# Kernel tuning notes

Measured on AMD Instinct MI355X. Metric: run time of the kernel, lower is better.

The kernel has to match this reference:

```python
import jax, jax.numpy as jnp
import numpy as np

NUM_HEADS = 12
DIM = 768
HEAD_DIM = DIM // NUM_HEADS
NUM_BUCKETS = 32
MAX_DISTANCE = 128
ELEV_SCALE = 1000.0


def _bucket_positions(relative_position):
    # Faithful port of RelativePositionBias2D._bucket_positions (torch .long() truncates;
    # values passed through the large branch are non-negative so astype(int32) matches).
    nb = NUM_BUCKETS // 2  # 16
    n = -relative_position
    ret = (n < 0).astype(jnp.int32) * nb
    n = jnp.abs(n)
    max_exact = nb // 2  # 8
    is_small = n < max_exact
    n_safe = jnp.maximum(n, 1).astype(jnp.float32)  # avoid log(0); masked by is_small
    val_if_large = max_exact + (
        jnp.log(n_safe / max_exact) / np.float32(np.log(MAX_DISTANCE / max_exact)) * (nb - max_exact)
    ).astype(jnp.int32)
    val_if_large = jnp.minimum(val_if_large, nb - 1)
    return ret + jnp.where(is_small, n, val_if_large)


def _bucket_idx(coords_2d):
    # coords_2d: [B, N, 2] in [0,1] -> integer grid coords
    coords_int = (coords_2d * MAX_DISTANCE).astype(jnp.int32)
    rel_x = coords_int[:, :, None, 0] - coords_int[:, None, :, 0]  # [B,N,N]
    rel_y = coords_int[:, :, None, 1] - coords_int[:, None, :, 1]
    bx = _bucket_positions(rel_x)
    by = _bucket_positions(rel_y)
    return bx * NUM_BUCKETS + by  # [B,N,N] int32 in [0, 1024)


def setup_inputs() -> dict:
    key = jax.random.key(0)
    ks = jax.random.split(key, 8)
    B, N, D = 4, 1024, DIM
    x = jax.random.normal(ks[0], (B, N, D), dtype=jnp.float32)
    coords_2d = jax.random.uniform(ks[1], (B, N, 2), dtype=jnp.float32)
    elevation_patches = jax.random.normal(ks[2], (B, N), dtype=jnp.float32) * 2000.0  # meters
    qkv_w = jax.random.normal(ks[3], (3 * D, D), dtype=jnp.float32) * 0.02
    qkv_b = jnp.zeros((3 * D,), dtype=jnp.float32)
    proj_w = jax.random.normal(ks[4], (D, D), dtype=jnp.float32) * 0.02
    proj_b = jnp.zeros((D,), dtype=jnp.float32)
    bias_table = jax.random.normal(ks[5], (NUM_BUCKETS * NUM_BUCKETS, NUM_HEADS), dtype=jnp.float32) * 0.02
    alpha = jnp.full((1,), 2.0, dtype=jnp.float32)
    return {"x": x, "coords_2d": coords_2d, "elevation_patches": elevation_patches,
            "qkv_w": qkv_w, "qkv_b": qkv_b, "proj_w": proj_w, "proj_b": proj_b,
            "bias_table": bias_table, "alpha": alpha}


def reference(x, coords_2d, elevation_patches, qkv_w, qkv_b, proj_w, proj_b, bias_table, alpha):
    B, N, D = x.shape
    H, hd = NUM_HEADS, HEAD_DIM
    scale = hd ** -0.5

    qkv = x @ qkv_w.T + qkv_b  # [B,N,3D]
    qkv = qkv.reshape(B, N, 3, H, hd)
    q = qkv[:, :, 0].transpose(0, 2, 1, 3)  # [B,H,N,hd]
    k = qkv[:, :, 1].transpose(0, 2, 1, 3)
    v = qkv[:, :, 2].transpose(0, 2, 1, 3)

    attn = jnp.einsum('bhnd,bhmd->bhnm', q * scale, k)  # [B,H,N,N]

    # relative position bias: gather from table, [B,N,N,H] -> [B,H,N,N]
    idx = _bucket_idx(coords_2d)
    rel_bias = bias_table[idx].transpose(0, 3, 1, 2)
    attn = attn + rel_bias

    # elevation bias: [B,N,N], broadcast over heads
    elev_diff = (elevation_patches[:, None, :] - elevation_patches[:, :, None]) / ELEV_SCALE
    elev_bias = jnp.clip(-alpha[0] * jax.nn.relu(elev_diff), -10.0, 0.0)
    attn = attn + elev_bias[:, None, :, :]

    attn = jax.nn.softmax(attn.astype(jnp.float32), axis=-1).astype(q.dtype)

    out = jnp.einsum('bhnm,bhmd->bhnd', attn, v)  # [B,H,N,hd]
    out = out.transpose(0, 2, 1, 3).reshape(B, N, D)
    return out @ proj_w.T + proj_b
```

## Files before the change

kernel.cpp:

```cpp
#include <hip/hip_runtime.h>
#include <hip/hip_bf16.h>
#include <math.h>

#define NH 12
#define HD 64
#define NSEQ 1024
#define DMODEL 768
#define LOG2E 1.44269504f

#if defined(__has_builtin)
#if __has_builtin(__builtin_amdgcn_permlane32_swap) && __has_builtin(__builtin_amdgcn_permlane16_swap)
#define USE_PLSWAP 1
#endif
#endif

typedef unsigned short ushort_t;
typedef float f32x4 __attribute__((ext_vector_type(4)));
typedef short bf16x8 __attribute__((ext_vector_type(8)));

__device__ __forceinline__ ushort_t f2bf(float f) {
    unsigned int u = __float_as_uint(f);
    u += 0x7FFFu + ((u >> 16) & 1u);
    return (ushort_t)(u >> 16);
}

__device__ __forceinline__ unsigned pk2(float x, float y) {
    __hip_bfloat162 t = __float22bfloat162_rn(make_float2(x, y));
    union { __hip_bfloat162 b; unsigned u; } c; c.b = t;
    return c.u;
}

__device__ __forceinline__ void gl_lds16(const ushort_t* g, ushort_t* l) {
    __builtin_amdgcn_global_load_lds(
        (const __attribute__((address_space(1))) unsigned int*)g,
        (__attribute__((address_space(3))) unsigned int*)l, 16, 0, 0);
}

#define XB_N   3145728u
#define WQB_N  1769472u
#define PWB_N  589824u
#define CVT_BLOCKS 2688

__device__ __forceinline__ int bucketf(int rel) {
    const int n = -rel;
    const int u = (n < 0) ? 16 : 0;
    const int a = n < 0 ? -n : n;
    if (a < 8) return u + a;
    int v = 8 + (int)(log2f((float)a * 0.125f) * 2.0f + 1e-4f);
    if (v > 15) v = 15;
    return u + v;
}

__global__ __launch_bounds__(256) void prep_kernel(
    const float* __restrict__ x, const float* __restrict__ w1,
    const float* __restrict__ w2, ushort_t* __restrict__ dst,
    const float* __restrict__ coords, const float* __restrict__ elev,
    const float* __restrict__ alpha_p, unsigned* __restrict__ pack)
{
    const int t = threadIdx.x;
    if (blockIdx.x < CVT_BLOCKS) {
        const unsigned i = blockIdx.x * 256 + t;
        const unsigned n0 = XB_N / 8, n1 = n0 + WQB_N / 8, n2 = n1 + PWB_N / 8;
        if (i >= n2) return;
        const float* src; unsigned off;
        if (i < n0)      { src = x;  off = i; }
        else if (i < n1) { src = w1; off = i - n0; }
        else             { src = w2; off = i - n1; }
        const float4 a = ((const float4*)src)[off * 2];
        const float4 b = ((const float4*)src)[off * 2 + 1];
        uint4 pk;
        pk.x = pk2(a.x, a.y); pk.y = pk2(a.z, a.w);
        pk.z = pk2(b.x, b.y); pk.w = pk2(b.z, b.w);
        ((uint4*)dst)[i] = pk;
    } else {
        const int blk = blockIdx.x - CVT_BLOCKS;
        const int b = blk >> 10, i = blk & 1023;
        const float alpha = alpha_p[0];
        const float2 ci = *(const float2*)&coords[(size_t)(b * NSEQ + i) * 2];
        const int cxi = (int)(ci.x * 128.0f), cyi = (int)(ci.y * 128.0f);
        const float ei = elev[b * NSEQ + i];
        const int j0 = t * 4;
        const float4 c01 = *(const float4*)&coords[(size_t)(b * NSEQ + j0) * 2];
        const float4 c23 = *(const float4*)&coords[(size_t)(b * NSEQ + j0 + 2) * 2];
        const float4 ej4 = *(const float4*)&elev[b * NSEQ + j0];
        const float cjx[4] = {c01.x, c01.z, c23.x, c23.z};
        const float cjy[4] = {c01.y, c01.w, c23.y, c23.w};
        const float ejv[4] = {ej4.x, ej4.y, ej4.z, ej4.w};
        unsigned r[4];
        #pragma unroll
        for (int k = 0; k < 4; ++k) {
            const int bx = bucketf(cxi - (int)(cjx[k] * 128.0f));
            const int by = bucketf(cyi - (int)(cjy[k] * 128.0f));
            const int idx = (bx << 5) + by;
            const float ed = (ejv[k] - ei) * 1e-3f;
            const float eb = fmaxf(-alpha * fmaxf(ed, 0.0f), -10.0f) * LOG2E;
            r[k] = ((unsigned)f2bf(eb) << 16) | (unsigned)idx;
        }
        uint4 o; o.x = r[0]; o.y = r[1]; o.z = r[2]; o.w = r[3];
        *(uint4*)&pack[((size_t)b << 20) + (size_t)i * NSEQ + j0] = o;
    }
}

__global__ __launch_bounds__(256) void qkv_gemm(
    const ushort_t* __restrict__ A, const ushort_t* __restrict__ B,
    const float* __restrict__ bias,
    ushort_t* __restrict__ Qb, ushort_t* __restrict__ Kb, ushort_t* __restrict__ Vtb)
{
    __shared__ __align__(16) ushort_t SM[6144];
    ushort_t* Asb = SM;
    ushort_t* Bsb = SM + 4096;
    const int t = threadIdx.x;
    const int lane = t & 63, w = t >> 6;
    const int wr = w >> 1, wc = w & 1;
    const int col = lane & 15, quad = lane >> 4;
    const int m0 = blockIdx.y * 128, c0 = blockIdx.x * 64;

    const f32x4 zero = {0.f, 0.f, 0.f, 0.f};
    f32x4 acc[4][2];
    #pragma unroll
    for (int i = 0; i < 4; ++i)
        #pragma unroll
        for (int j = 0; j < 2; ++j) acc[i][j] = zero;

    const int arow = w * 32 + (lane >> 2);
    const int brow = w * 16 + (lane >> 2);
    const int scol = (lane & 3) * 8;
    const ushort_t* Ag = A + (size_t)(m0 + arow) * DMODEL + scol;
    const ushort_t* Bg = B + (size_t)(c0 + brow) * DMODEL + scol;
    ushort_t* Asw = Asb + w * 32 * 32;
    ushort_t* Bsw = Bsb + w * 16 * 32;

    for (int k0 = 0; k0 < DMODEL; k0 += 32) {
        __syncthreads();
        gl_lds16(Ag + k0, Asw);
        gl_lds16(Ag + (size_t)16 * DMODEL + k0, Asw + 16 * 32);
        gl_lds16(Bg + k0, Bsw);
        __syncthreads();
        bf16x8 af[4], bf[2];
        #pragma unroll
        for (int im = 0; im < 4; ++im)
            af[im] = *(const bf16x8*)&Asb[(wr * 64 + im * 16 + col) * 32 + quad * 8];
        #pragma unroll
        for (int jn = 0; jn < 2; ++jn)
            bf[jn] = *(const bf16x8*)&Bsb[(wc * 32 + jn * 16 + col) * 32 + quad * 8];
        #pragma unroll
        for (int im = 0; im < 4; ++im)
            #pragma unroll
            for (int jn = 0; jn < 2; ++jn)
                acc[im][jn] = __builtin_amdgcn_mfma_f32_16x16x32_bf16(af[im], bf[jn], acc[im][jn], 0, 0, 0);
    }

    const int s = c0 / DMODEL;
    const int h = (c0 % DMODEL) >> 6;
    const int b = m0 >> 10;
    const int bh = b * NH + h;
    const int n0 = (m0 & (NSEQ - 1)) + wr * 64;
    const int d0 = (c0 & 63);
    const int cb = c0 + wc * 32;

    __syncthreads();

    if (s < 2) {
        ushort_t* lt = SM + w * 1280;
        ushort_t* dst = (s == 0) ? Qb : Kb;
        const float sc = (s == 0) ? 0.125f * LOG2E : 1.0f;
        float bv[2];
        #pragma unroll
        for (int jn = 0; jn < 2; ++jn) bv[jn] = bias[cb + jn * 16 + col];
        const int row16 = lane >> 2, seg = lane & 3;
        #pragma unroll
        for (int im = 0; im < 4; ++im) {
            #pragma unroll
            for (int jn = 0; jn < 2; ++jn) {
                const f32x4 a = acc[im][jn];
                #pragma unroll
                for (int r = 0; r < 4; ++r)
                    lt[(quad * 4 + r) * 40 + jn * 16 + col] = f2bf((a[r] + bv[jn]) * sc);
            }
            const uint4 u0 = *(const uint4*)&lt[row16 * 40 + seg * 8];
            const size_t gb = ((size_t)bh * NSEQ + n0 + im * 16 + row16) * HD
                            + wc * 32 + seg * 8;
            *(uint4*)&dst[gb] = u0;
        }
    } else {
        #pragma unroll
        for (int im = 0; im < 4; ++im) {
            #pragma unroll
            for (int jn = 0; jn < 2; ++jn) {
                const int d = wc * 32 + jn * 16 + col;
                const float bvv = bias[cb + jn * 16 + col];
                const f32x4 a = acc[im][jn];
                uint2 p;
                p.x = pk2(a[0] + bvv, a[1] + bvv);
                p.y = pk2(a[2] + bvv, a[3] + bvv);
                *(uint2*)&Vtb[((size_t)bh * HD + d) * NSEQ + n0 + im * 16 + quad * 4] = p;
            }
        }
    }
    (void)d0;
}

__global__ __launch_bounds__(256) void attn_mfma(
    const ushort_t* __restrict__ Qb, const ushort_t* __restrict__ Kb,
    const ushort_t* __restrict__ Vtb,
    const unsigned* __restrict__ pack,
    const float* __restrict__ table,
    ushort_t* __restrict__ Ob)
{
    __shared__ __align__(16) ushort_t Ks[2][64 * 72];
    __shared__ __align__(16) ushort_t Vt[2][64 * 72];
#if !USE_PLSWAP
    __shared__ __align__(16) ushort_t Ps[64 * 72];
#endif
    __shared__ ushort_t tabu[1024];

    const int t = threadIdx.x;
    const int lane = t & 63, w = t >> 6;
    const int col = lane & 15, quad = lane >> 4;
    const int bid = blockIdx.x;
    const int it = bid & 15, bh = bid >> 4;
    const int h = bh % NH, b = bh / NH;
    const int i0 = it * 64;

    for (int i = t; i < 1024; i += 256)
        tabu[i] = f2bf(table[i * NH + h] * LOG2E);

    const ushort_t* Qg = Qb + ((size_t)bh * NSEQ + i0 + w * 16 + col) * HD;
    const bf16x8 aq0 = *(const bf16x8*)(Qg + quad * 8);
    const bf16x8 aq1 = *(const bf16x8*)(Qg + 32 + quad * 8);

    const size_t kvbase = (size_t)bh * NSEQ * HD;
    const unsigned* prow = pack + ((size_t)b << 20)
                         + (size_t)(i0 + w * 16 + col) * NSEQ + quad * 4;

    const int srow = t >> 3, sc8 = (t & 7) * 8;
    const int so0 = srow * 72 + sc8;
    const int so1 = (srow + 32) * 72 + sc8;

    uint4 k0 = *(const uint4*)&Kb[kvbase + (size_t)srow * HD + sc8];
    uint4 k1 = *(const uint4*)&Kb[kvbase + (size_t)(srow + 32) * HD + sc8];
    uint4 v0 = *(const uint4*)&Vtb[kvbase + (size_t)srow * NSEQ + sc8];
    uint4 v1 = *(const uint4*)&Vtb[kvbase + (size_t)(srow + 32) * NSEQ + sc8];
    *(uint4*)&Ks[0][so0] = k0;
    *(uint4*)&Ks[0][so1] = k1;
    *(uint4*)&Vt[0][so0] = v0;
    *(uint4*)&Vt[0][so1] = v1;
    k0 = *(const uint4*)&Kb[kvbase + (size_t)(64 + srow) * HD + sc8];
    k1 = *(const uint4*)&Kb[kvbase + (size_t)(64 + srow + 32) * HD + sc8];
    v0 = *(const uint4*)&Vtb[kvbase + (size_t)srow * NSEQ + 64 + sc8];
    v1 = *(const uint4*)&Vtb[kvbase + (size_t)(srow + 32) * NSEQ + 64 + sc8];

    const f32x4 zero = {0.f, 0.f, 0.f, 0.f};
    f32x4 o_acc[4];
    #pragma unroll
    for (int i = 0; i < 4; ++i) o_acc[i] = zero;
    float l_l = 0.f;

    #pragma unroll 2
    for (int jt = 0; jt < 16; ++jt) {
        __syncthreads();
        const int cur = jt & 1;
        const int j0 = jt * 64;

        if (jt < 15) {
            *(uint4*)&Ks[cur ^ 1][so0] = k0;
            *(uint4*)&Ks[cur ^ 1][so1] = k1;
            *(uint4*)&Vt[cur ^ 1][so0] = v0;
            *(uint4*)&Vt[cur ^ 1][so1] = v1;
        }
        if (jt < 14) {
            const int j2 = (jt + 2) * 64;
            k0 = *(const uint4*)&Kb[kvbase + (size_t)(j2 + srow) * HD + sc8];
            k1 = *(const uint4*)&Kb[kvbase + (size_t)(j2 + srow + 32) * HD + sc8];
            v0 = *(const uint4*)&Vtb[kvbase + (size_t)srow * NSEQ + j2 + sc8];
            v1 = *(const uint4*)&Vtb[kvbase + (size_t)(srow + 32) * NSEQ + j2 + sc8];
        }
        uint4 pk4[4];
        #pragma unroll
        for (int jb = 0; jb < 4; ++jb)
            pk4[jb] = *(const uint4*)(prow + j0 + jb * 16);

        f32x4 sacc[4];
        #pragma unroll
        for (int jb = 0; jb < 4; ++jb) {
            sacc[jb] = zero;
            const bf16x8 kb0 = *(const bf16x8*)&Ks[cur][(jb * 16 + col) * 72 + quad * 8];
            const bf16x8 kb1 = *(const bf16x8*)&Ks[cur][(jb * 16 + col) * 72 + 32 + quad * 8];
            sacc[jb] = __builtin_amdgcn_mfma_f32_16x16x32_bf16(kb0, aq0, sacc[jb], 0, 0, 0);
            sacc[jb] = __builtin_amdgcn_mfma_f32_16x16x32_bf16(kb1, aq1, sacc[jb], 0, 0, 0);
        }

        float rbeb[4][4];
        #pragma unroll
        for (int jb = 0; jb < 4; ++jb) {
            const uint4 pkv = pk4[jb];
            rbeb[jb][0] = __uint_as_float((unsigned)tabu[pkv.x & 1023u] << 16) + __uint_as_float(pkv.x & 0xFFFF0000u);
            rbeb[jb][1] = __uint_as_float((unsigned)tabu[pkv.y & 1023u] << 16) + __uint_as_float(pkv.y & 0xFFFF0000u);
            rbeb[jb][2] = __uint_as_float((unsigned)tabu[pkv.z & 1023u] << 16) + __uint_as_float(pkv.z & 0xFFFF0000u);
            rbeb[jb][3] = __uint_as_float((unsigned)tabu[pkv.w & 1023u] << 16) + __uint_as_float(pkv.w & 0xFFFF0000u);
        }

        float psum = 0.f;
        unsigned Wd[4][2];
        #pragma unroll
        for (int jb = 0; jb < 4; ++jb) {
            const float p0 = exp2f(sacc[jb][0] + rbeb[jb][0]);
            const float p1 = exp2f(sacc[jb][1] + rbeb[jb][1]);
            const float p2 = exp2f(sacc[jb][2] + rbeb[jb][2]);
            const float p3 = exp2f(sacc[jb][3] + rbeb[jb][3]);
            psum += (p0 + p1) + (p2 + p3);
            Wd[jb][0] = pk2(p0, p1);
            Wd[jb][1] = pk2(p2, p3);
        }
        l_l += psum;

        bf16x8 ap0, ap1;
#if USE_PLSWAP
        {
            union { unsigned u[4]; bf16x8 b; } A0, A1;
            #pragma unroll
            for (int j1 = 0; j1 < 2; ++j1) {
                #pragma unroll
                for (int v = 0; v < 2; ++v) {
                    auto h1 = __builtin_amdgcn_permlane32_swap(
                        Wd[2 * j1][v], Wd[2 * j1 + 1][v], false, false);
                    auto h2 = __builtin_amdgcn_permlane16_swap(
                        h1[0], h1[1], false, false);
                    if (j1 == 0) { A0.u[0 + v] = h2[0]; A0.u[2 + v] = h2[1]; }
                    else         { A1.u[0 + v] = h2[0]; A1.u[2 + v] = h2[1]; }
                }
            }
            ap0 = A0.b;
            ap1 = A1.b;
        }
#else
        #pragma unroll
        for (int jb = 0; jb < 4; ++jb) {
            uint2 st;
            st.x = Wd[jb][0];
            st.y = Wd[jb][1];
            *(uint2*)&Ps[(w * 16 + col) * 72 + jb * 16 + quad * 4] = st;
        }
        ap0 = *(const bf16x8*)&Ps[(w * 16 + col) * 72 + quad * 8];
        ap1 = *(const bf16x8*)&Ps[(w * 16 + col) * 72 + 32 + quad * 8];
#endif

        #pragma unroll
        for (int db = 0; db < 4; ++db) {
            const bf16x8 vv0 = *(const bf16x8*)&Vt[cur][(db * 16 + col) * 72 + quad * 8];
            const bf16x8 vv1 = *(const bf16x8*)&Vt[cur][(db * 16 + col) * 72 + 32 + quad * 8];
            o_acc[db] = __builtin_amdgcn_mfma_f32_16x16x32_bf16(ap0, vv0, o_acc[db], 0, 0, 0);
            o_acc[db] = __builtin_amdgcn_mfma_f32_16x16x32_bf16(ap1, vv1, o_acc[db], 0, 0, 0);
        }
    }

    float l = l_l;
    l += __shfl_xor(l, 16);
    l += __shfl_xor(l, 32);
    #pragma unroll
    for (int r = 0; r < 4; ++r) {
        const float lr = __shfl(l, w * 16 + quad * 4 + r);
        const float inv = 1.f / lr;
        const int ri = w * 16 + quad * 4 + r;
        const size_t base = ((size_t)(b * NSEQ) + i0 + ri) * DMODEL + h * HD;
        #pragma unroll
        for (int db = 0; db < 4; ++db)
            Ob[base + db * 16 + col] = f2bf(o_acc[db][r] * inv);
    }
}

__global__ __launch_bounds__(256) void proj_gemm(
    const ushort_t* __restrict__ A, const ushort_t* __restrict__ B,
    const float* __restrict__ bias, float* __restrict__ out)
{
    __shared__ __align__(16) ushort_t As[64 * 32];
    __shared__ __align__(16) ushort_t Bs[64 * 32];
    const int t = threadIdx.x;
    const int lane = t & 63, w = t >> 6;
    const int wr = w >> 1, wc = w & 1;
    const int col = lane & 15, quad = lane >> 4;
    const int m0 = blockIdx.y * 64, c0 = blockIdx.x * 64;

    const f32x4 zero = {0.f, 0.f, 0.f, 0.f};
    f32x4 acc[2][2];
    #pragma unroll
    for (int i = 0; i < 2; ++i)
        #pragma unroll
        for (int j = 0; j < 2; ++j) acc[i][j] = zero;

    const int srow = w * 16 + (lane >> 2);
    const int scol = (lane & 3) * 8;
    const ushort_t* Ag = A + (size_t)(m0 + srow) * DMODEL + scol;
    const ushort_t* Bg = B + (size_t)(c0 + srow) * DMODEL + scol;
    ushort_t* Asw = &As[w * 16 * 32];
    ushort_t* Bsw = &Bs[w * 16 * 32];

    for (int k0 = 0; k0 < DMODEL; k0 += 32) {
        __syncthreads();
        gl_lds16(Ag + k0, Asw);
        gl_lds16(Bg + k0, Bsw);
        __syncthreads();
        bf16x8 af[2], bf[2];
        #pragma unroll
        for (int im = 0; im < 2; ++im)
            af[im] = *(const bf16x8*)&As[(wr * 32 + im * 16 + col) * 32 + quad * 8];
        #pragma unroll
        for (int jn = 0; jn < 2; ++jn)
            bf[jn] = *(const bf16x8*)&Bs[(wc * 32 + jn * 16 + col) * 32 + quad * 8];
        #pragma unroll
        for (int im = 0; im < 2; ++im)
            #pragma unroll
            for (int jn = 0; jn < 2; ++jn)
                acc[im][jn] = __builtin_amdgcn_mfma_f32_16x16x32_bf16(af[im], bf[jn], acc[im][jn], 0, 0, 0);
    }

    #pragma unroll
    for (int im = 0; im < 2; ++im) {
        #pragma unroll
        for (int jn = 0; jn < 2; ++jn) {
            const int c = c0 + wc * 32 + jn * 16 + col;
            const float bv = bias[c];
            #pragma unroll
            for (int r = 0; r < 4; ++r) {
                const int m = m0 + wr * 32 + im * 16 + quad * 4 + r;
                out[(size_t)m * DMODEL + c] = acc[im][jn][r] + bv;
            }
        }
    }
}

extern "C" void kernel_launch(void* const* d_in, const int* in_sizes, int n_in,
                              void* d_out, int out_size, void* d_ws, size_t ws_size,
                              hipStream_t stream) {
    const float* x       = (const float*)d_in[0];
    const float* coords  = (const float*)d_in[1];
    const float* elev    = (const float*)d_in[2];
    const float* qkv_w   = (const float*)d_in[3];
    const float* qkv_b   = (const float*)d_in[4];
    const float* proj_w  = (const float*)d_in[5];
    const float* proj_b  = (const float*)d_in[6];
    const float* btable  = (const float*)d_in[7];
    const float* alpha   = (const float*)d_in[8];
    float* out = (float*)d_out;

    ushort_t* wsu = (ushort_t*)d_ws;
    ushort_t* xb  = wsu;
    ushort_t* wqb = wsu + 3145728;
    ushort_t* pwb = wsu + 4915200;
    ushort_t* Qb  = wsu + 5505024;
    ushort_t* Kb  = wsu + 8650752;
    ushort_t* Vtb = wsu + 11796480;
    ushort_t* Ob  = wsu + 14942208;
    unsigned* pck = (unsigned*)(wsu + 18087936);

    prep_kernel<<<CVT_BLOCKS + 4096, 256, 0, stream>>>(
        x, qkv_w, proj_w, wsu, coords, elev, alpha, pck);
    qkv_gemm<<<dim3(36, 32), 256, 0, stream>>>(xb, wqb, qkv_b, Qb, Kb, Vtb);
    attn_mfma<<<768, 256, 0, stream>>>(Qb, Kb, Vtb, pck, btable, Ob);
    proj_gemm<<<dim3(12, 64), 256, 0, stream>>>(Ob, pwb, proj_b, out);
}
```

Before: 191.8 us.

## Split attention key range across two wave groups per block with LDS reduction

The attention kernel now launches 512 threads per block. Two groups of four waves each process half of the key/value sequence for the same 64 query rows, using their own double-buffered LDS tiles. At the end, the partial outputs and row sums are combined through LDS before normalisation. The goal is more waves in flight and a shorter serial loop per wave, in exchange for more LDS, an extra reduction step and dropping the non-permlane fallback path.

```diff
diff --git a/kernel.cpp b/kernel.cpp
--- a/kernel.cpp
+++ b/kernel.cpp
@@ -7,12 +7,6 @@
 #define NSEQ 1024
 #define DMODEL 768
 #define LOG2E 1.44269504f
-
-#if defined(__has_builtin)
-#if __has_builtin(__builtin_amdgcn_permlane32_swap) && __has_builtin(__builtin_amdgcn_permlane16_swap)
-#define USE_PLSWAP 1
-#endif
-#endif
 
 typedef unsigned short ushort_t;
 typedef float f32x4 __attribute__((ext_vector_type(4)));
@@ -200,55 +194,55 @@
     (void)d0;
 }
 
-__global__ __launch_bounds__(256) void attn_mfma(
+__global__ __launch_bounds__(512) void attn_mfma(
     const ushort_t* __restrict__ Qb, const ushort_t* __restrict__ Kb,
     const ushort_t* __restrict__ Vtb,
     const unsigned* __restrict__ pack,
     const float* __restrict__ table,
     ushort_t* __restrict__ Ob)
 {
-    __shared__ __align__(16) ushort_t Ks[2][64 * 72];
-    __shared__ __align__(16) ushort_t Vt[2][64 * 72];
-#if !USE_PLSWAP
-    __shared__ __align__(16) ushort_t Ps[64 * 72];
-#endif
+    __shared__ __align__(16) ushort_t Ks[2][2][64 * 72];
+    __shared__ __align__(16) ushort_t Vt[2][2][64 * 72];
     __shared__ ushort_t tabu[1024];
 
     const int t = threadIdx.x;
     const int lane = t & 63, w = t >> 6;
+    const int g = w >> 2, wg = w & 3;
     const int col = lane & 15, quad = lane >> 4;
     const int bid = blockIdx.x;
     const int it = bid & 15, bh = bid >> 4;
     const int h = bh % NH, b = bh / NH;
     const int i0 = it * 64;
 
-    for (int i = t; i < 1024; i += 256)
+    for (int i = t; i < 1024; i += 512)
         tabu[i] = f2bf(table[i * NH + h] * LOG2E);
 
-    const ushort_t* Qg = Qb + ((size_t)bh * NSEQ + i0 + w * 16 + col) * HD;
+    const ushort_t* Qg = Qb + ((size_t)bh * NSEQ + i0 + wg * 16 + col) * HD;
     const bf16x8 aq0 = *(const bf16x8*)(Qg + quad * 8);
     const bf16x8 aq1 = *(const bf16x8*)(Qg + 32 + quad * 8);
 
     const size_t kvbase = (size_t)bh * NSEQ * HD;
     const unsigned* prow = pack + ((size_t)b << 20)
-                         + (size_t)(i0 + w * 16 + col) * NSEQ + quad * 4;
-
-    const int srow = t >> 3, sc8 = (t & 7) * 8;
+                         + (size_t)(i0 + wg * 16 + col) * NSEQ + quad * 4;
+
+    const int tg = t & 255;
+    const int srow = tg >> 3, sc8 = (tg & 7) * 8;
     const int so0 = srow * 72 + sc8;
     const int so1 = (srow + 32) * 72 + sc8;
-
-    uint4 k0 = *(const uint4*)&Kb[kvbase + (size_t)srow * HD + sc8];
-    uint4 k1 = *(const uint4*)&Kb[kvbase + (size_t)(srow + 32) * HD + sc8];
-    uint4 v0 = *(const uint4*)&Vtb[kvbase + (size_t)srow * NSEQ + sc8];
-    uint4 v1 = *(const uint4*)&Vtb[kvbase + (size_t)(srow + 32) * NSEQ + sc8];
-    *(uint4*)&Ks[0][so0] = k0;
-    *(uint4*)&Ks[0][so1] = k1;
-    *(uint4*)&Vt[0][so0] = v0;
-    *(uint4*)&Vt[0][so1] = v1;
-    k0 = *(const uint4*)&Kb[kvbase + (size_t)(64 + srow) * HD + sc8];
-    k1 = *(const uint4*)&Kb[kvbase + (size_t)(64 + srow + 32) * HD + sc8];
-    v0 = *(const uint4*)&Vtb[kvbase + (size_t)srow * NSEQ + 64 + sc8];
-    v1 = *(const uint4*)&Vtb[kvbase + (size_t)(srow + 32) * NSEQ + 64 + sc8];
+    const int r0 = g * 512;
+
+    uint4 k0 = *(const uint4*)&Kb[kvbase + (size_t)(r0 + srow) * HD + sc8];
+    uint4 k1 = *(const uint4*)&Kb[kvbase + (size_t)(r0 + srow + 32) * HD + sc8];
+    uint4 v0 = *(const uint4*)&Vtb[kvbase + (size_t)srow * NSEQ + r0 + sc8];
+    uint4 v1 = *(const uint4*)&Vtb[kvbase + (size_t)(srow + 32) * NSEQ + r0 + sc8];
+    *(uint4*)&Ks[g][0][so0] = k0;
+    *(uint4*)&Ks[g][0][so1] = k1;
+    *(uint4*)&Vt[g][0][so0] = v0;
+    *(uint4*)&Vt[g][0][so1] = v1;
+    k0 = *(const uint4*)&Kb[kvbase + (size_t)(r0 + 64 + srow) * HD + sc8];
+    k1 = *(const uint4*)&Kb[kvbase + (size_t)(r0 + 64 + srow + 32) * HD + sc8];
+    v0 = *(const uint4*)&Vtb[kvbase + (size_t)srow * NSEQ + r0 + 64 + sc8];
+    v1 = *(const uint4*)&Vtb[kvbase + (size_t)(srow + 32) * NSEQ + r0 + 64 + sc8];
 
     const f32x4 zero = {0.f, 0.f, 0.f, 0.f};
     f32x4 o_acc[4];
@@ -257,19 +251,19 @@
     float l_l = 0.f;
 
     #pragma unroll 2
-    for (int jt = 0; jt < 16; ++jt) {
+    for (int s = 0; s < 8; ++s) {
         __syncthreads();
-        const int cur = jt & 1;
-        const int j0 = jt * 64;
-
-        if (jt < 15) {
-            *(uint4*)&Ks[cur ^ 1][so0] = k0;
-            *(uint4*)&Ks[cur ^ 1][so1] = k1;
-            *(uint4*)&Vt[cur ^ 1][so0] = v0;
-            *(uint4*)&Vt[cur ^ 1][so1] = v1;
-        }
-        if (jt < 14) {
-            const int j2 = (jt + 2) * 64;
+        const int cur = s & 1;
+        const int j0 = r0 + s * 64;
+
+        if (s < 7) {
+            *(uint4*)&Ks[g][cur ^ 1][so0] = k0;
+            *(uint4*)&Ks[g][cur ^ 1][so1] = k1;
+            *(uint4*)&Vt[g][cur ^ 1][so0] = v0;
+            *(uint4*)&Vt[g][cur ^ 1][so1] = v1;
+        }
+        if (s < 6) {
+            const int j2 = r0 + (s + 2) * 64;
             k0 = *(const uint4*)&Kb[kvbase + (size_t)(j2 + srow) * HD + sc8];
             k1 = *(const uint4*)&Kb[kvbase + (size_t)(j2 + srow + 32) * HD + sc8];
             v0 = *(const uint4*)&Vtb[kvbase + (size_t)srow * NSEQ + j2 + sc8];
@@ -284,8 +278,8 @@
         #pragma unroll
         for (int jb = 0; jb < 4; ++jb) {
             sacc[jb] = zero;
-            const bf16x8 kb0 = *(const bf16x8*)&Ks[cur][(jb * 16 + col) * 72 + quad * 8];
-            const bf16x8 kb1 = *(const bf16x8*)&Ks[cur][(jb * 16 + col) * 72 + 32 + quad * 8];
+            const bf16x8 kb0 = *(const bf16x8*)&Ks[g][cur][(jb * 16 + col) * 72 + quad * 8];
+            const bf16x8 kb1 = *(const bf16x8*)&Ks[g][cur][(jb * 16 + col) * 72 + 32 + quad * 8];
             sacc[jb] = __builtin_amdgcn_mfma_f32_16x16x32_bf16(kb0, aq0, sacc[jb], 0, 0, 0);
             sacc[jb] = __builtin_amdgcn_mfma_f32_16x16x32_bf16(kb1, aq1, sacc[jb], 0, 0, 0);
         }
@@ -315,7 +309,6 @@
         l_l += psum;
 
         bf16x8 ap0, ap1;
-#if USE_PLSWAP
         {
             union { unsigned u[4]; bf16x8 b; } A0, A1;
             #pragma unroll
@@ -333,22 +326,11 @@
             ap0 = A0.b;
             ap1 = A1.b;
         }
-#else
-        #pragma unroll
-        for (int jb = 0; jb < 4; ++jb) {
-            uint2 st;
-            st.x = Wd[jb][0];
-            st.y = Wd[jb][1];
-            *(uint2*)&Ps[(w * 16 + col) * 72 + jb * 16 + quad * 4] = st;
-        }
-        ap0 = *(const bf16x8*)&Ps[(w * 16 + col) * 72 + quad * 8];
-        ap1 = *(const bf16x8*)&Ps[(w * 16 + col) * 72 + 32 + quad * 8];
-#endif
 
         #pragma unroll
         for (int db = 0; db < 4; ++db) {
-            const bf16x8 vv0 = *(const bf16x8*)&Vt[cur][(db * 16 + col) * 72 + quad * 8];
-            const bf16x8 vv1 = *(const bf16x8*)&Vt[cur][(db * 16 + col) * 72 + 32 + quad * 8];
+            const bf16x8 vv0 = *(const bf16x8*)&Vt[g][cur][(db * 16 + col) * 72 + quad * 8];
+            const bf16x8 vv1 = *(const bf16x8*)&Vt[g][cur][(db * 16 + col) * 72 + 32 + quad * 8];
             o_acc[db] = __builtin_amdgcn_mfma_f32_16x16x32_bf16(ap0, vv0, o_acc[db], 0, 0, 0);
             o_acc[db] = __builtin_amdgcn_mfma_f32_16x16x32_bf16(ap1, vv1, o_acc[db], 0, 0, 0);
         }
@@ -357,15 +339,32 @@
     float l = l_l;
     l += __shfl_xor(l, 16);
     l += __shfl_xor(l, 32);
-    #pragma unroll
-    for (int r = 0; r < 4; ++r) {
-        const float lr = __shfl(l, w * 16 + quad * 4 + r);
-        const float inv = 1.f / lr;
-        const int ri = w * 16 + quad * 4 + r;
-        const size_t base = ((size_t)(b * NSEQ) + i0 + ri) * DMODEL + h * HD;
+
+    __syncthreads();
+    float* Ored = (float*)&Ks[0][0][0];
+    float* lred = (float*)&Vt[0][0][0];
+    if (g == 1) {
         #pragma unroll
         for (int db = 0; db < 4; ++db)
-            Ob[base + db * 16 + col] = f2bf(o_acc[db][r] * inv);
+            #pragma unroll
+            for (int r = 0; r < 4; ++r)
+                Ored[(wg * 16 + quad * 4 + r) * 68 + db * 16 + col] = o_acc[db][r];
+        if (quad == 0) lred[wg * 16 + col] = l;
+    }
+    __syncthreads();
+    if (g == 0) {
+        #pragma unroll
+        for (int r = 0; r < 4; ++r) {
+            const int ri = wg * 16 + quad * 4 + r;
+            const float lr = __shfl(l, wg * 16 + quad * 4 + r) + lred[ri];
+            const float inv = 1.f / lr;
+            const size_t base = ((size_t)(b * NSEQ) + i0 + ri) * DMODEL + h * HD;
+            #pragma unroll
+            for (int db = 0; db < 4; ++db) {
+                const float ov = o_acc[db][r] + Ored[ri * 68 + db * 16 + col];
+                Ob[base + db * 16 + col] = f2bf(ov * inv);
+            }
+        }
     }
 }
 
@@ -456,6 +455,6 @@
     prep_kernel<<<CVT_BLOCKS + 4096, 256, 0, stream>>>(
         x, qkv_w, proj_w, wsu, coords, elev, alpha, pck);
     qkv_gemm<<<dim3(36, 32), 256, 0, stream>>>(xb, wqb, qkv_b, Qb, Kb, Vtb);
-    attn_mfma<<<768, 256, 0, stream>>>(Qb, Kb, Vtb, pck, btable, Ob);
+    attn_mfma<<<768, 512, 0, stream>>>(Qb, Kb, Vtb, pck, btable, Ob);
     proj_gemm<<<dim3(12, 64), 256, 0, stream>>>(Ob, pwb, proj_b, out);
 }
```

Result: slower. 200.1 us (+4.3%).
